# Performance work log

Hardware: AMD Instinct MI355X
Metric: run time of the kernel (lower is better)

## Reference

```python
import jax, jax.numpy as jnp
import numpy as np
import math

D_MODEL = 1024
NUM_HEADS = 16
HEAD_DIM = D_MODEL // NUM_HEADS
EPS = 1e-6
ROPE_BASE = 10000.0


def _rope_cos_sin(seq_len, dim, dtype):
    inv_freq = 1.0 / (ROPE_BASE ** (jnp.arange(0, dim, 2, dtype=jnp.float32) / dim))
    t = jnp.arange(seq_len, dtype=jnp.float32)
    freqs = jnp.outer(t, inv_freq)                 # [s, dim/2]
    emb = jnp.concatenate([freqs, freqs], axis=-1)  # [s, dim]
    return jnp.cos(emb).astype(dtype), jnp.sin(emb).astype(dtype)


def _rotate_half(x):
    x1, x2 = jnp.split(x, 2, axis=-1)
    return jnp.concatenate([-x2, x1], axis=-1)


def setup_inputs() -> dict:
    key = jax.random.key(0)
    k1, k2, k3 = jax.random.split(key, 3)
    b, s = 2, 2048
    x = jax.random.normal(k1, (b, s, D_MODEL), dtype=jnp.float32)
    norm_w = jnp.ones((D_MODEL,), dtype=jnp.float32)
    qkv_w = jax.random.normal(k2, (3 * D_MODEL, D_MODEL), dtype=jnp.float32) * (1.0 / math.sqrt(D_MODEL))
    qkv_b = jnp.zeros((3 * D_MODEL,), dtype=jnp.float32)
    proj_w = jax.random.normal(k3, (D_MODEL, D_MODEL), dtype=jnp.float32) * (1.0 / math.sqrt(D_MODEL))
    proj_b = jnp.zeros((D_MODEL,), dtype=jnp.float32)
    return {"x": x, "norm_w": norm_w, "qkv_w": qkv_w, "qkv_b": qkv_b,
            "proj_w": proj_w, "proj_b": proj_b}


def reference(x, norm_w, qkv_w, qkv_b, proj_w, proj_b):
    b, s, d = x.shape
    # RMSNorm (pre-LN)
    xn = x * jax.lax.rsqrt(jnp.mean(x * x, axis=-1, keepdims=True) + EPS) * norm_w
    # Fused QKV
    qkv = jnp.einsum('bsd,ed->bse', xn, qkv_w) + qkv_b
    q, k, v = jnp.split(qkv, 3, axis=-1)
    # [b, h, s, hd]
    def shape(t):
        return t.reshape(b, s, NUM_HEADS, HEAD_DIM).transpose(0, 2, 1, 3)
    q, k, v = shape(q), shape(k), shape(v)
    # RoPE on head_dim
    cos, sin = _rope_cos_sin(s, HEAD_DIM, x.dtype)  # [s, hd]
    q = q * cos + _rotate_half(q) * sin
    k = k * cos + _rotate_half(k) * sin
    # Naive causal attention
    scale = 1.0 / math.sqrt(HEAD_DIM)
    scores = jnp.einsum('bhqd,bhkd->bhqk', q, k) * scale
    causal = jnp.tril(jnp.ones((s, s), dtype=bool))
    scores = jnp.where(causal, scores, -jnp.inf)
    attn = jax.nn.softmax(scores, axis=-1)
    y = jnp.einsum('bhqk,bhkd->bhqd', attn, v)
    y = y.transpose(0, 2, 1, 3).reshape(b, s, d)
    return jnp.einsum('bsd,ed->bse', y, proj_w) + proj_b
```

## Files before the change

### kernel.cpp

```cpp
#include <hip/hip_runtime.h>
#include <cstdint>
#include <cstddef>

#define NB 2
#define NS 2048
#define ND 1024
#define NH 16
#define HD 64
#define ROWS 4096
#define E3 3072

using bf16 = __bf16;
typedef __attribute__((ext_vector_type(4))) __bf16 bf16x4;
typedef __attribute__((ext_vector_type(8))) __bf16 bf16x8;
typedef __attribute__((ext_vector_type(4))) float f32x4;

__device__ __forceinline__ f32x4 mfma16(bf16x8 a, bf16x8 b, f32x4 c) {
    return __builtin_amdgcn_mfma_f32_16x16x32_bf16(a, b, c, 0, 0, 0);
}

__device__ __forceinline__ void gll16(const bf16* src, bf16* lds) {
    __builtin_amdgcn_global_load_lds(
        (const __attribute__((address_space(1))) void*)src,
        (__attribute__((address_space(3))) void*)lds, 16, 0, 0);
}

__global__ __launch_bounds__(256) void cast_f32_bf16(const float* __restrict__ in,
                                                     bf16* __restrict__ out, int n) {
    int i = (blockIdx.x * 256 + threadIdx.x) * 4;
    if (i + 3 < n) {
        float4 v = *(const float4*)(in + i);
        bf16x4 o;
        o[0] = (bf16)v.x; o[1] = (bf16)v.y; o[2] = (bf16)v.z; o[3] = (bf16)v.w;
        *(bf16x4*)(out + i) = o;
    }
}

__global__ __launch_bounds__(256) void rmsnorm_cast(const float* __restrict__ x,
                                                    const float* __restrict__ w,
                                                    bf16* __restrict__ xn) {
    int row = blockIdx.x;
    int tid = threadIdx.x;
    const float* xr = x + (size_t)row * ND;
    float4 v = ((const float4*)xr)[tid];
    float ss = v.x*v.x + v.y*v.y + v.z*v.z + v.w*v.w;
    #pragma unroll
    for (int m = 32; m >= 1; m >>= 1) ss += __shfl_xor(ss, m);
    __shared__ float wsum[4];
    if ((tid & 63) == 0) wsum[tid >> 6] = ss;
    __syncthreads();
    float total = wsum[0] + wsum[1] + wsum[2] + wsum[3];
    float scale = rsqrtf(total * (1.0f / ND) + 1e-6f);
    float4 wv = ((const float4*)w)[tid];
    bf16x4 o;
    o[0] = (bf16)(v.x * scale * wv.x);
    o[1] = (bf16)(v.y * scale * wv.y);
    o[2] = (bf16)(v.z * scale * wv.z);
    o[3] = (bf16)(v.w * scale * wv.w);
    ((bf16x4*)(xn + (size_t)row * ND))[tid] = o;
}

__global__ __launch_bounds__(256) void gemm_qkv_rope(const bf16* __restrict__ A,
                                                     const bf16* __restrict__ Bm,
                                                     const float* __restrict__ bias,
                                                     bf16* __restrict__ Qb,
                                                     bf16* __restrict__ Kb,
                                                     bf16* __restrict__ Vraw) {
    const int K = ND;
    __shared__ bf16 Asm[128 * 32];
    __shared__ bf16 Bsm[128 * 32];
    const int tid = threadIdx.x;
    const int wave = tid >> 6, lane = tid & 63;
    const int quad = lane >> 4, l15 = lane & 15;
    const int row0 = blockIdx.x * 128, col0 = blockIdx.y * 128;
    const int wr = (wave >> 1) * 64, wc = (wave & 1) * 64;
    const int srow = lane >> 2;
    const int scol = (lane & 3) * 8;

    f32x4 acc[4][4] = {};

    for (int k0 = 0; k0 < K; k0 += 32) {
        #pragma unroll
        for (int i = 0; i < 2; ++i) {
            int r = wave * 32 + i * 16;
            gll16(A + (size_t)(row0 + r + srow) * K + k0 + scol, Asm + r * 32);
            gll16(Bm + (size_t)(col0 + r + srow) * K + k0 + scol, Bsm + r * 32);
        }
        __syncthreads();
        bf16x8 af[4], bff[4];
        #pragma unroll
        for (int t = 0; t < 4; ++t) {
            af[t]  = *(const bf16x8*)(Asm + (wr + t * 16 + l15) * 32 + quad * 8);
            bff[t] = *(const bf16x8*)(Bsm + (wc + t * 16 + l15) * 32 + quad * 8);
        }
        #pragma unroll
        for (int mt = 0; mt < 4; ++mt)
            #pragma unroll
            for (int nt = 0; nt < 4; ++nt)
                acc[mt][nt] = mfma16(af[mt], bff[nt], acc[mt][nt]);
        __syncthreads();
    }

    float bb[4];
    #pragma unroll
    for (int nt = 0; nt < 4; ++nt) bb[nt] = bias[col0 + wc + nt * 16 + l15];

    const int region = col0 >> 10;
    if (region == 2) {
        int cv = col0 - 2048 + wc;
        #pragma unroll
        for (int mt = 0; mt < 4; ++mt)
            #pragma unroll
            for (int r = 0; r < 4; ++r) {
                int row = row0 + wr + mt * 16 + quad * 4 + r;
                #pragma unroll
                for (int nt = 0; nt < 4; ++nt)
                    Vraw[(size_t)row * ND + cv + nt * 16 + l15] = (bf16)(acc[mt][nt][r] + bb[nt]);
            }
    } else {
        const float scale = (region == 0) ? 0.125f : 1.0f;
        bf16* Ob = (region == 0) ? Qb : Kb;
        const int h = ((col0 + wc) & 1023) >> 6;
        float freq0 = powf(10000.0f, -(float)l15 * (1.0f / 32.0f));
        float freq1 = powf(10000.0f, -(float)(16 + l15) * (1.0f / 32.0f));
        #pragma unroll
        for (int mt = 0; mt < 4; ++mt) {
            #pragma unroll
            for (int r = 0; r < 4; ++r) {
                int row = row0 + wr + mt * 16 + quad * 4 + r;
                int s = row & (NS - 1);
                int b = row >> 11;
                float sn0, c0, sn1, c1;
                sincosf((float)s * freq0, &sn0, &c0);
                sincosf((float)s * freq1, &sn1, &c1);
                size_t obase = ((size_t)(b * NH + h) * NS + s) * 64;
                #pragma unroll
                for (int nt = 0; nt < 4; ++nt) {
                    float v  = acc[mt][nt][r] + bb[nt];
                    float vp = acc[mt][nt ^ 2][r] + bb[nt ^ 2];
                    float cc = (nt & 1) ? c1 : c0;
                    float ss = (nt & 1) ? sn1 : sn0;
                    float res = (nt < 2) ? (v * cc - vp * ss) : (v * cc + vp * ss);
                    Ob[obase + nt * 16 + l15] = (bf16)(res * scale);
                }
            }
        }
    }
}

__global__ __launch_bounds__(256) void gemm_bt_f32(const bf16* __restrict__ A,
                                                   const bf16* __restrict__ Bm,
                                                   const float* __restrict__ bias,
                                                   float* __restrict__ C,
                                                   int M, int N, int K) {
    __shared__ bf16 Asm[128 * 32];
    __shared__ bf16 Bsm[128 * 32];
    const int tid = threadIdx.x;
    const int wave = tid >> 6, lane = tid & 63;
    const int quad = lane >> 4, l15 = lane & 15;
    const int row0 = blockIdx.x * 128, col0 = blockIdx.y * 128;
    const int wr = (wave >> 1) * 64, wc = (wave & 1) * 64;
    const int srow = lane >> 2;
    const int scol = (lane & 3) * 8;

    f32x4 acc[4][4] = {};

    for (int k0 = 0; k0 < K; k0 += 32) {
        #pragma unroll
        for (int i = 0; i < 2; ++i) {
            int r = wave * 32 + i * 16;
            gll16(A + (size_t)(row0 + r + srow) * K + k0 + scol, Asm + r * 32);
            gll16(Bm + (size_t)(col0 + r + srow) * K + k0 + scol, Bsm + r * 32);
        }
        __syncthreads();
        bf16x8 af[4], bff[4];
        #pragma unroll
        for (int t = 0; t < 4; ++t) {
            af[t]  = *(const bf16x8*)(Asm + (wr + t * 16 + l15) * 32 + quad * 8);
            bff[t] = *(const bf16x8*)(Bsm + (wc + t * 16 + l15) * 32 + quad * 8);
        }
        #pragma unroll
        for (int mt = 0; mt < 4; ++mt)
            #pragma unroll
            for (int nt = 0; nt < 4; ++nt)
                acc[mt][nt] = mfma16(af[mt], bff[nt], acc[mt][nt]);
        __syncthreads();
    }

    #pragma unroll
    for (int nt = 0; nt < 4; ++nt) {
        int col = col0 + wc + nt * 16 + l15;
        float bv = bias[col];
        #pragma unroll
        for (int mt = 0; mt < 4; ++mt) {
            int row = row0 + wr + mt * 16 + quad * 4;
            #pragma unroll
            for (int r = 0; r < 4; ++r)
                C[(size_t)(row + r) * N + col] = acc[mt][nt][r] + bv;
        }
    }
}

__global__ __launch_bounds__(256) void transpose_v(const bf16* __restrict__ Vraw,
                                                   bf16* __restrict__ Vt) {
    __shared__ bf16 t[64][65];
    int bid = blockIdx.x;
    int st = bid & 31;
    int bh = bid >> 5;
    int h = bh & 15, b = bh >> 4;
    int s0 = st * 64;
    int d = threadIdx.x & 63, i0 = threadIdx.x >> 6;
    for (int i = i0; i < 64; i += 4)
        t[i][d] = Vraw[(size_t)(b * NS + s0 + i) * ND + h * 64 + d];
    __syncthreads();
    int j = threadIdx.x & 63, d0 = threadIdx.x >> 6;
    int jp = (j & 32) | ((j & 12) << 1) | ((j & 16) >> 2) | (j & 3);
    for (int dd = d0; dd < 64; dd += 4)
        Vt[((size_t)bh * 64 + dd) * NS + s0 + jp] = t[j][dd];
}

__global__ __launch_bounds__(256) void attn(const bf16* __restrict__ Q,
                                            const bf16* __restrict__ K,
                                            const bf16* __restrict__ Vt,
                                            bf16* __restrict__ Y) {
    __shared__ bf16 Ksm[4096];
    __shared__ bf16 Vsm[4096];
    int bid = blockIdx.x;
    int g = bid >> 5;
    int bh = bid & 31;
    int qt = (g < 8) ? (15 - g) : (g - 8);
    int tid = threadIdx.x;
    int wave = tid >> 6, lane = tid & 63;
    int quad = lane >> 4, l15 = lane & 15;
    int q0 = qt * 128 + wave * 32;
    const bf16* Qh = Q + (size_t)bh * NS * 64;
    const bf16* Kh = K + (size_t)bh * NS * 64;
    const bf16* Vh = Vt + (size_t)bh * 64 * NS;
    const float NEG_INF = -__builtin_inff();

    const int srow = tid >> 3;
    const int sx   = (tid & 7) ^ (srow & 7);
    const bf16* sK = Kh + (size_t)srow * 64 + sx * 8;
    const bf16* sV = Vh + (size_t)srow * NS + sx * 8;
    bf16* dK = Ksm + wave * 512;
    bf16* dV = Vsm + wave * 512;

    const int x7 = l15 & 7;
    const bf16* pk0 = Ksm + l15 * 64 + ((quad) ^ x7) * 8;
    const bf16* pk1 = Ksm + l15 * 64 + ((4 + quad) ^ x7) * 8;
    const bf16* pv0 = Vsm + l15 * 64 + ((quad) ^ x7) * 8;
    const bf16* pv1 = Vsm + l15 * 64 + ((4 + quad) ^ x7) * 8;

    bf16x8 bq[2][2];
    #pragma unroll
    for (int t = 0; t < 2; ++t)
        #pragma unroll
        for (int hh = 0; hh < 2; ++hh)
            bq[t][hh] = *(const bf16x8*)(Qh + (size_t)(q0 + t * 16 + l15) * 64 + hh * 32 + quad * 8);

    f32x4 o[2][4] = {};
    float lsum[2] = {0.f, 0.f};

    const int ncb = 2 * (qt + 1);
    for (int c = 0; c < ncb; ++c) {
        const int kb = c * 64;
        const bf16* kSrc = sK + (size_t)kb * 64;
        const bf16* vSrc = sV + kb;
        gll16(kSrc, dK);
        gll16(kSrc + 32 * 64, dK + 2048);
        gll16(vSrc, dV);
        gll16(vSrc + (size_t)32 * NS, dV + 2048);
        __syncthreads();

        #pragma unroll
        for (int ksub = 0; ksub < 2; ++ksub) {
            const int kbs = kb + ksub * 32;
            if (kbs <= q0) {
                const int kh0 = ksub * 2;
                bf16x8 ak00 = *(const bf16x8*)(pk0 + kh0 * 1024);
                bf16x8 ak01 = *(const bf16x8*)(pk1 + kh0 * 1024);
                bf16x8 ak10 = *(const bf16x8*)(pk0 + (kh0 + 1) * 1024);
                bf16x8 ak11 = *(const bf16x8*)(pk1 + (kh0 + 1) * 1024);
                const bf16* pv = ksub ? pv1 : pv0;
                bf16x8 vf0 = *(const bf16x8*)(pv);
                bf16x8 vf1 = *(const bf16x8*)(pv + 1024);
                bf16x8 vf2 = *(const bf16x8*)(pv + 2048);
                bf16x8 vf3 = *(const bf16x8*)(pv + 3072);
                const bool masked = (kbs == q0);
                #pragma unroll
                for (int t = 0; t < 2; ++t) {
                    f32x4 sh0 = {}, sh1 = {};
                    sh0 = mfma16(ak00, bq[t][0], sh0);
                    sh0 = mfma16(ak01, bq[t][1], sh0);
                    sh1 = mfma16(ak10, bq[t][0], sh1);
                    sh1 = mfma16(ak11, bq[t][1], sh1);
                    if (masked) {
                        int qy = q0 + t * 16 + l15;
                        #pragma unroll
                        for (int r = 0; r < 4; ++r) {
                            if (kbs + quad * 4 + r > qy)      sh0[r] = NEG_INF;
                            if (kbs + 16 + quad * 4 + r > qy) sh1[r] = NEG_INF;
                        }
                    }
                    bf16x8 pa;
                    float ls = 0.f;
                    #pragma unroll
                    for (int j = 0; j < 4; ++j) {
                        float p0 = __expf(sh0[j]);
                        float p1 = __expf(sh1[j]);
                        ls += p0 + p1;
                        pa[j] = (bf16)p0;
                        pa[4 + j] = (bf16)p1;
                    }
                    lsum[t] += ls;
                    o[t][0] = mfma16(pa, vf0, o[t][0]);
                    o[t][1] = mfma16(pa, vf1, o[t][1]);
                    o[t][2] = mfma16(pa, vf2, o[t][2]);
                    o[t][3] = mfma16(pa, vf3, o[t][3]);
                }
            }
        }
        __syncthreads();
    }

    int b = bh >> 4, h = bh & 15;
    #pragma unroll
    for (int t = 0; t < 2; ++t) {
        float red = lsum[t];
        red += __shfl_xor(red, 16);
        red += __shfl_xor(red, 32);
        #pragma unroll
        for (int r = 0; r < 4; ++r) {
            float il = 1.0f / __shfl(red, quad * 4 + r);
            size_t row = (size_t)(b * NS + q0 + t * 16 + quad * 4 + r);
            #pragma unroll
            for (int nt = 0; nt < 4; ++nt)
                Y[row * ND + h * 64 + nt * 16 + l15] = (bf16)(o[t][nt][r] * il);
        }
    }
}

extern "C" void kernel_launch(void* const* d_in, const int* in_sizes, int n_in,
                              void* d_out, int out_size, void* d_ws, size_t ws_size,
                              hipStream_t stream) {
    const float* x      = (const float*)d_in[0];
    const float* norm_w = (const float*)d_in[1];
    const float* qkv_w  = (const float*)d_in[2];
    const float* qkv_b  = (const float*)d_in[3];
    const float* proj_w = (const float*)d_in[4];
    const float* proj_b = (const float*)d_in[5];
    float* out = (float*)d_out;

    char* ws = (char*)d_ws;
    size_t off = 0;
    bf16* xn   = (bf16*)(ws + off); off += (size_t)ROWS * ND * 2;
    bf16* wq   = (bf16*)(ws + off); off += (size_t)E3 * ND * 2;
    bf16* wp   = (bf16*)(ws + off); off += (size_t)ND * ND * 2;
    bf16* Qb   = (bf16*)(ws + off); off += (size_t)NB * NH * NS * HD * 2;
    bf16* Kb   = (bf16*)(ws + off); off += (size_t)NB * NH * NS * HD * 2;
    bf16* Vraw = (bf16*)(ws + off); off += (size_t)ROWS * ND * 2;
    bf16* Vt   = (bf16*)(ws + off); off += (size_t)NB * NH * HD * NS * 2;
    bf16* Y    = (bf16*)(ws + off); off += (size_t)ROWS * ND * 2;

    cast_f32_bf16<<<3072, 256, 0, stream>>>(qkv_w, wq, E3 * ND);
    cast_f32_bf16<<<1024, 256, 0, stream>>>(proj_w, wp, ND * ND);
    rmsnorm_cast<<<ROWS, 256, 0, stream>>>(x, norm_w, xn);
    gemm_qkv_rope<<<dim3(ROWS / 128, E3 / 128), 256, 0, stream>>>(xn, wq, qkv_b, Qb, Kb, Vraw);
    transpose_v<<<NB * NH * (NS / 64), 256, 0, stream>>>(Vraw, Vt);
    attn<<<NB * NH * (NS / 128), 256, 0, stream>>>(Qb, Kb, Vt, Y);
    gemm_bt_f32<<<dim3(ROWS / 128, ND / 128), 256, 0, stream>>>(Y, wp, proj_b, out, ROWS, ND, ND);
}
```

Before: 201.5 us.

## Fuse V transpose into QKV epilogue, double-buffer attention, precompute RoPE table

Several changes at once. The V transpose kernel is folded into the QKV GEMM epilogue, which now writes V straight into the transposed [b,h,d,s] layout with permuted 4-element stores. The attention kernel now stages 128-key blocks into double-buffered LDS so the next block loads while the current one computes. RoPE sin/cos values move into a precomputed table kernel, and the two weight-cast launches are merged into one. The aim is to cut launches, an extra round trip through global memory for V, and per-element transcendental work. The cost is doubled LDS use in attention, which may lower occupancy.

Result: no change. 198.7 us (-1.4%).

```diff
diff --git a/kernel.cpp b/kernel.cpp
--- a/kernel.cpp
+++ b/kernel.cpp
@@ -25,15 +25,27 @@
         (__attribute__((address_space(3))) void*)lds, 16, 0, 0);
 }
 
-__global__ __launch_bounds__(256) void cast_f32_bf16(const float* __restrict__ in,
-                                                     bf16* __restrict__ out, int n) {
+__global__ __launch_bounds__(256) void rope_table(float4* __restrict__ tab) {
+    int idx = blockIdx.x * 256 + threadIdx.x;
+    int s = idx >> 4, j = idx & 15;
+    float f0 = powf(10000.0f, -(float)j * (1.0f / 32.0f));
+    float f1 = powf(10000.0f, -(float)(j + 16) * (1.0f / 32.0f));
+    float sn0, c0, sn1, c1;
+    sincosf((float)s * f0, &sn0, &c0);
+    sincosf((float)s * f1, &sn1, &c1);
+    tab[idx] = make_float4(c0, sn0, c1, sn1);
+}
+
+__global__ __launch_bounds__(256) void cast_weights(const float* __restrict__ qkv_w,
+                                                    const float* __restrict__ proj_w,
+                                                    bf16* __restrict__ wq) {
+    const int n1 = E3 * ND;
     int i = (blockIdx.x * 256 + threadIdx.x) * 4;
-    if (i + 3 < n) {
-        float4 v = *(const float4*)(in + i);
-        bf16x4 o;
-        o[0] = (bf16)v.x; o[1] = (bf16)v.y; o[2] = (bf16)v.z; o[3] = (bf16)v.w;
-        *(bf16x4*)(out + i) = o;
-    }
+    const float* src = (i < n1) ? (qkv_w + i) : (proj_w + (i - n1));
+    float4 v = *(const float4*)src;
+    bf16x4 o;
+    o[0] = (bf16)v.x; o[1] = (bf16)v.y; o[2] = (bf16)v.z; o[3] = (bf16)v.w;
+    *(bf16x4*)(wq + i) = o;
 }
 
 __global__ __launch_bounds__(256) void rmsnorm_cast(const float* __restrict__ x,
@@ -63,9 +75,10 @@
 __global__ __launch_bounds__(256) void gemm_qkv_rope(const bf16* __restrict__ A,
                                                      const bf16* __restrict__ Bm,
                                                      const float* __restrict__ bias,
+                                                     const float4* __restrict__ tab,
                                                      bf16* __restrict__ Qb,
                                                      bf16* __restrict__ Kb,
-                                                     bf16* __restrict__ Vraw) {
+                                                     bf16* __restrict__ Vt) {
     const int K = ND;
     __shared__ bf16 Asm[128 * 32];
     __shared__ bf16 Bsm[128 * 32];
@@ -107,22 +120,27 @@
 
     const int region = col0 >> 10;
     if (region == 2) {
-        int cv = col0 - 2048 + wc;
-        #pragma unroll
-        for (int mt = 0; mt < 4; ++mt)
-            #pragma unroll
-            for (int r = 0; r < 4; ++r) {
-                int row = row0 + wr + mt * 16 + quad * 4 + r;
+        const int cv = col0 - 2048 + wc;
+        const int h = cv >> 6;
+        const int b = row0 >> 11;
+        const int sloc = row0 & (NS - 1);
+        #pragma unroll
+        for (int nt = 0; nt < 4; ++nt) {
+            const int d = nt * 16 + l15;
+            bf16* vrow = Vt + ((size_t)(b * NH + h) * 64 + d) * NS;
+            #pragma unroll
+            for (int mt = 0; mt < 4; ++mt) {
+                int sp = sloc + wr + (mt >> 1) * 32 + quad * 8 + (mt & 1) * 4;
+                bf16x4 o4;
                 #pragma unroll
-                for (int nt = 0; nt < 4; ++nt)
-                    Vraw[(size_t)row * ND + cv + nt * 16 + l15] = (bf16)(acc[mt][nt][r] + bb[nt]);
+                for (int r = 0; r < 4; ++r) o4[r] = (bf16)(acc[mt][nt][r] + bb[nt]);
+                *(bf16x4*)(vrow + sp) = o4;
             }
+        }
     } else {
         const float scale = (region == 0) ? 0.125f : 1.0f;
         bf16* Ob = (region == 0) ? Qb : Kb;
         const int h = ((col0 + wc) & 1023) >> 6;
-        float freq0 = powf(10000.0f, -(float)l15 * (1.0f / 32.0f));
-        float freq1 = powf(10000.0f, -(float)(16 + l15) * (1.0f / 32.0f));
         #pragma unroll
         for (int mt = 0; mt < 4; ++mt) {
             #pragma unroll
@@ -130,16 +148,14 @@
                 int row = row0 + wr + mt * 16 + quad * 4 + r;
                 int s = row & (NS - 1);
                 int b = row >> 11;
-                float sn0, c0, sn1, c1;
-                sincosf((float)s * freq0, &sn0, &c0);
-                sincosf((float)s * freq1, &sn1, &c1);
+                float4 cs = tab[s * 16 + l15];
                 size_t obase = ((size_t)(b * NH + h) * NS + s) * 64;
                 #pragma unroll
                 for (int nt = 0; nt < 4; ++nt) {
                     float v  = acc[mt][nt][r] + bb[nt];
                     float vp = acc[mt][nt ^ 2][r] + bb[nt ^ 2];
-                    float cc = (nt & 1) ? c1 : c0;
-                    float ss = (nt & 1) ? sn1 : sn0;
+                    float cc = (nt & 1) ? cs.z : cs.x;
+                    float ss = (nt & 1) ? cs.w : cs.y;
                     float res = (nt < 2) ? (v * cc - vp * ss) : (v * cc + vp * ss);
                     Ob[obase + nt * 16 + l15] = (bf16)(res * scale);
                 }
@@ -201,30 +217,12 @@
     }
 }
 
-__global__ __launch_bounds__(256) void transpose_v(const bf16* __restrict__ Vraw,
-                                                   bf16* __restrict__ Vt) {
-    __shared__ bf16 t[64][65];
-    int bid = blockIdx.x;
-    int st = bid & 31;
-    int bh = bid >> 5;
-    int h = bh & 15, b = bh >> 4;
-    int s0 = st * 64;
-    int d = threadIdx.x & 63, i0 = threadIdx.x >> 6;
-    for (int i = i0; i < 64; i += 4)
-        t[i][d] = Vraw[(size_t)(b * NS + s0 + i) * ND + h * 64 + d];
-    __syncthreads();
-    int j = threadIdx.x & 63, d0 = threadIdx.x >> 6;
-    int jp = (j & 32) | ((j & 12) << 1) | ((j & 16) >> 2) | (j & 3);
-    for (int dd = d0; dd < 64; dd += 4)
-        Vt[((size_t)bh * 64 + dd) * NS + s0 + jp] = t[j][dd];
-}
-
 __global__ __launch_bounds__(256) void attn(const bf16* __restrict__ Q,
                                             const bf16* __restrict__ K,
                                             const bf16* __restrict__ Vt,
                                             bf16* __restrict__ Y) {
-    __shared__ bf16 Ksm[4096];
-    __shared__ bf16 Vsm[4096];
+    __shared__ bf16 Ksm[2][8192];
+    __shared__ bf16 Vsm[2][8192];
     int bid = blockIdx.x;
     int g = bid >> 5;
     int bh = bid & 31;
@@ -238,18 +236,19 @@
     const bf16* Vh = Vt + (size_t)bh * 64 * NS;
     const float NEG_INF = -__builtin_inff();
 
-    const int srow = tid >> 3;
-    const int sx   = (tid & 7) ^ (srow & 7);
-    const bf16* sK = Kh + (size_t)srow * 64 + sx * 8;
-    const bf16* sV = Vh + (size_t)srow * NS + sx * 8;
-    bf16* dK = Ksm + wave * 512;
-    bf16* dV = Vsm + wave * 512;
-
-    const int x7 = l15 & 7;
-    const bf16* pk0 = Ksm + l15 * 64 + ((quad) ^ x7) * 8;
-    const bf16* pk1 = Ksm + l15 * 64 + ((4 + quad) ^ x7) * 8;
-    const bf16* pv0 = Vsm + l15 * 64 + ((quad) ^ x7) * 8;
-    const bf16* pv1 = Vsm + l15 * 64 + ((4 + quad) ^ x7) * 8;
+    const int krow = wave * 8 + (lane >> 3);
+    const int ksx  = (lane & 7) ^ (krow & 7);
+    const bf16* sK = Kh + (size_t)krow * 64 + ksx * 8;
+    const int vrow = wave * 4 + (lane >> 4);
+    const int vcx  = (lane & 15) ^ (vrow & 15);
+    const bf16* sV = Vh + (size_t)vrow * NS + vcx * 8;
+
+    const bf16* pk0 = &Ksm[0][l15 * 64 + ((quad) ^ (l15 & 7)) * 8];
+    const bf16* pk1 = &Ksm[0][l15 * 64 + ((4 + quad) ^ (l15 & 7)) * 8];
+    const bf16* pvk[4];
+    #pragma unroll
+    for (int ks = 0; ks < 4; ++ks)
+        pvk[ks] = &Vsm[0][l15 * 128 + ((ks * 4 + quad) ^ l15) * 8];
 
     bf16x8 bq[2][2];
     #pragma unroll
@@ -261,31 +260,33 @@
     f32x4 o[2][4] = {};
     float lsum[2] = {0.f, 0.f};
 
-    const int ncb = 2 * (qt + 1);
-    for (int c = 0; c < ncb; ++c) {
-        const int kb = c * 64;
-        const bf16* kSrc = sK + (size_t)kb * 64;
-        const bf16* vSrc = sV + kb;
-        gll16(kSrc, dK);
-        gll16(kSrc + 32 * 64, dK + 2048);
-        gll16(vSrc, dV);
-        gll16(vSrc + (size_t)32 * NS, dV + 2048);
-        __syncthreads();
-
-        #pragma unroll
-        for (int ksub = 0; ksub < 2; ++ksub) {
+    auto stage = [&](int c, int par) {
+        const int kb = c * 128;
+        bf16* dK = &Ksm[par][wave * 512];
+        bf16* dV = &Vsm[par][wave * 512];
+        #pragma unroll
+        for (int i = 0; i < 4; ++i)
+            gll16(sK + (size_t)(kb + i * 32) * 64, dK + i * 2048);
+        #pragma unroll
+        for (int i = 0; i < 4; ++i)
+            gll16(sV + kb + (size_t)(i * 16) * NS, dV + i * 2048);
+    };
+
+    auto compute = [&](int cc, int par) {
+        const int kb = cc * 128;
+        const int pb = par * 8192;
+        #pragma unroll
+        for (int ksub = 0; ksub < 4; ++ksub) {
             const int kbs = kb + ksub * 32;
             if (kbs <= q0) {
-                const int kh0 = ksub * 2;
-                bf16x8 ak00 = *(const bf16x8*)(pk0 + kh0 * 1024);
-                bf16x8 ak01 = *(const bf16x8*)(pk1 + kh0 * 1024);
-                bf16x8 ak10 = *(const bf16x8*)(pk0 + (kh0 + 1) * 1024);
-                bf16x8 ak11 = *(const bf16x8*)(pk1 + (kh0 + 1) * 1024);
-                const bf16* pv = ksub ? pv1 : pv0;
-                bf16x8 vf0 = *(const bf16x8*)(pv);
-                bf16x8 vf1 = *(const bf16x8*)(pv + 1024);
-                bf16x8 vf2 = *(const bf16x8*)(pv + 2048);
-                bf16x8 vf3 = *(const bf16x8*)(pv + 3072);
+                bf16x8 ak00 = *(const bf16x8*)(pk0 + pb + ksub * 2048);
+                bf16x8 ak01 = *(const bf16x8*)(pk1 + pb + ksub * 2048);
+                bf16x8 ak10 = *(const bf16x8*)(pk0 + pb + ksub * 2048 + 1024);
+                bf16x8 ak11 = *(const bf16x8*)(pk1 + pb + ksub * 2048 + 1024);
+                bf16x8 vf0 = *(const bf16x8*)(pvk[ksub] + pb);
+                bf16x8 vf1 = *(const bf16x8*)(pvk[ksub] + pb + 2048);
+                bf16x8 vf2 = *(const bf16x8*)(pvk[ksub] + pb + 4096);
+                bf16x8 vf3 = *(const bf16x8*)(pvk[ksub] + pb + 6144);
                 const bool masked = (kbs == q0);
                 #pragma unroll
                 for (int t = 0; t < 2; ++t) {
@@ -320,6 +321,15 @@
                 }
             }
         }
+    };
+
+    const int ncb = qt + 1;
+    stage(0, 0);
+    __syncthreads();
+    for (int c = 0; c < ncb; ++c) {
+        const int par = c & 1;
+        if (c + 1 < ncb) stage(c + 1, par ^ 1);
+        compute(c, par);
         __syncthreads();
     }
 
@@ -353,20 +363,19 @@
 
     char* ws = (char*)d_ws;
     size_t off = 0;
-    bf16* xn   = (bf16*)(ws + off); off += (size_t)ROWS * ND * 2;
-    bf16* wq   = (bf16*)(ws + off); off += (size_t)E3 * ND * 2;
-    bf16* wp   = (bf16*)(ws + off); off += (size_t)ND * ND * 2;
-    bf16* Qb   = (bf16*)(ws + off); off += (size_t)NB * NH * NS * HD * 2;
-    bf16* Kb   = (bf16*)(ws + off); off += (size_t)NB * NH * NS * HD * 2;
-    bf16* Vraw = (bf16*)(ws + off); off += (size_t)ROWS * ND * 2;
-    bf16* Vt   = (bf16*)(ws + off); off += (size_t)NB * NH * HD * NS * 2;
-    bf16* Y    = (bf16*)(ws + off); off += (size_t)ROWS * ND * 2;
-
-    cast_f32_bf16<<<3072, 256, 0, stream>>>(qkv_w, wq, E3 * ND);
-    cast_f32_bf16<<<1024, 256, 0, stream>>>(proj_w, wp, ND * ND);
+    bf16* xn    = (bf16*)(ws + off); off += (size_t)ROWS * ND * 2;
+    bf16* wq    = (bf16*)(ws + off); off += (size_t)E3 * ND * 2;
+    bf16* wp    = (bf16*)(ws + off); off += (size_t)ND * ND * 2;
+    bf16* Qb    = (bf16*)(ws + off); off += (size_t)NB * NH * NS * HD * 2;
+    bf16* Kb    = (bf16*)(ws + off); off += (size_t)NB * NH * NS * HD * 2;
+    bf16* Vt    = (bf16*)(ws + off); off += (size_t)NB * NH * HD * NS * 2;
+    bf16* Y     = (bf16*)(ws + off); off += (size_t)ROWS * ND * 2;
+    float4* tab = (float4*)(ws + off); off += (size_t)NS * 16 * sizeof(float4);
+
+    rope_table<<<NS * 16 / 256, 256, 0, stream>>>(tab);
+    cast_weights<<<(E3 * ND + ND * ND) / 1024, 256, 0, stream>>>(qkv_w, proj_w, wq);
     rmsnorm_cast<<<ROWS, 256, 0, stream>>>(x, norm_w, xn);
-    gemm_qkv_rope<<<dim3(ROWS / 128, E3 / 128), 256, 0, stream>>>(xn, wq, qkv_b, Qb, Kb, Vraw);
-    transpose_v<<<NB * NH * (NS / 64), 256, 0, stream>>>(Vraw, Vt);
+    gemm_qkv_rope<<<dim3(ROWS / 128, E3 / 128), 256, 0, stream>>>(xn, wq, qkv_b, tab, Qb, Kb, Vt);
     attn<<<NB * NH * (NS / 128), 256, 0, stream>>>(Qb, Kb, Vt, Y);
     gemm_bt_f32<<<dim3(ROWS / 128, ND / 128), 256, 0, stream>>>(Y, wp, proj_b, out, ROWS, ND, ND);
 }
```
